# Kernel tuning notes

Hardware: AMD Instinct MI355X
Metric: run time of the kernel (lower is better)

The kernel has to match this reference:

```python
import jax, jax.numpy as jnp
import numpy as np

INPUT_SIZE = 256
OUTPUT_SIZE = 128
N = 8192
SLOPE = 0.01
NEG_BIG = -9e15


def setup_inputs() -> dict:
    key = jax.random.key(0)
    k_h, k_adj, k_W, k_a = jax.random.split(key, 4)
    h = jax.random.normal(k_h, (N, INPUT_SIZE), dtype=jnp.float32)
    adj = jax.random.randint(k_adj, (N, N), 0, 2, dtype=jnp.int32)
    # xavier_uniform with gain=1.414
    gain = 1.414
    lim_W = gain * np.sqrt(6.0 / (INPUT_SIZE + OUTPUT_SIZE))
    W = jax.random.uniform(k_W, (INPUT_SIZE, OUTPUT_SIZE), dtype=jnp.float32, minval=-lim_W, maxval=lim_W)
    lim_a = gain * np.sqrt(6.0 / (2 * OUTPUT_SIZE + 1))
    a = jax.random.uniform(k_a, (2 * OUTPUT_SIZE, 1), dtype=jnp.float32, minval=-lim_a, maxval=lim_a)
    return {"h": h, "adj": adj, "W": W, "a": a}


def reference(h, adj, W, a):
    # Wh: [N, F]
    Wh = h @ W
    Fo = Wh.shape[1]
    # Original builds [N, N, 2F] concat then matmul with a; equivalent to
    # e[i, j] = leaky_relu(Wh[i] . a[:F] + Wh[j] . a[F:]) via broadcasting.
    src = Wh @ a[:Fo, 0]   # [N]
    dst = Wh @ a[Fo:, 0]   # [N]
    e = jax.nn.leaky_relu(src[:, None] + dst[None, :], negative_slope=SLOPE)  # [N, N]
    att = jnp.where(adj > 0, e, NEG_BIG)
    att = jax.nn.softmax(att, axis=1)
    return att @ Wh
```

## Files before the change

kernel.cpp:

```cpp
#include <hip/hip_runtime.h>
#include <hip/hip_bf16.h>

typedef unsigned short u16;
typedef unsigned int u32;
typedef __attribute__((ext_vector_type(8))) short short8;
typedef __attribute__((ext_vector_type(4))) float f32x4;

#define NN 8192
#define KIN 256
#define FOUT 128
#define SPLITS 8
#define KPER (NN / SPLITS)
#define BK 64
#define ITERS (KPER / BK)
#define L2E 1.4426950408889634f

__device__ __forceinline__ float exp2fast(float x) { return __builtin_amdgcn_exp2f(x); }

__device__ __forceinline__ u16 f2bf(float f) {
    u32 u = __float_as_uint(f);
    u32 r = ((u >> 16) & 1u) + 0x7fffu;
    return (u16)((u + r) >> 16);
}
__device__ __forceinline__ u32 pk_bf16(float a, float b) {
    union { __hip_bfloat162 h2; u32 u; } cv;
    cv.h2 = __float22bfloat162_rn(make_float2(a, b));
    return cv.u;
}
__device__ __forceinline__ u32 fkey(float f) {
    u32 b = __float_as_uint(f);
    return (b & 0x80000000u) ? ~b : (b | 0x80000000u);
}
__device__ __forceinline__ float funkey(u32 k) {
    u32 b = (k & 0x80000000u) ? (k & 0x7fffffffu) : ~k;
    return __uint_as_float(b);
}

__global__ __launch_bounds__(256) void k1_wh(
    const float* __restrict__ h, const float* __restrict__ W, const float* __restrict__ a,
    u16* __restrict__ whbt,
    float* __restrict__ src, float* __restrict__ dst, u32* __restrict__ gmaxk)
{
    __shared__ float hT[64][36];
    __shared__ u16   lt[128][40];
    __shared__ float sd[32][2];
    const int t  = threadIdx.x;
    const int m0 = blockIdx.x * 32;
    const int rq = t >> 5, cq = t & 31;

    float acc[4][4];
#pragma unroll
    for (int i = 0; i < 4; i++)
#pragma unroll
        for (int j = 0; j < 4; j++) acc[i][j] = 0.f;
    if (t < 64) sd[t >> 1][t & 1] = 0.f;

    for (int kt = 0; kt < KIN; kt += 64) {
        __syncthreads();
#pragma unroll
        for (int s2 = 0; s2 < 2; s2++) {
            int f = s2 * 256 + t;
            int r = f >> 4, kc = (f & 15) * 4;
            float4 hv = *(const float4*)(h + (size_t)(m0 + r) * KIN + kt + kc);
            hT[kc + 0][r] = hv.x; hT[kc + 1][r] = hv.y;
            hT[kc + 2][r] = hv.z; hT[kc + 3][r] = hv.w;
        }
        __syncthreads();
        for (int k = 0; k < 64; k++) {
            float4 wv = *(const float4*)(W + (size_t)(kt + k) * FOUT + cq * 4);
            float h0 = hT[k][rq * 4 + 0], h1 = hT[k][rq * 4 + 1];
            float h2 = hT[k][rq * 4 + 2], h3 = hT[k][rq * 4 + 3];
            acc[0][0] += h0 * wv.x; acc[0][1] += h0 * wv.y; acc[0][2] += h0 * wv.z; acc[0][3] += h0 * wv.w;
            acc[1][0] += h1 * wv.x; acc[1][1] += h1 * wv.y; acc[1][2] += h1 * wv.z; acc[1][3] += h1 * wv.w;
            acc[2][0] += h2 * wv.x; acc[2][1] += h2 * wv.y; acc[2][2] += h2 * wv.z; acc[2][3] += h2 * wv.w;
            acc[3][0] += h3 * wv.x; acc[3][1] += h3 * wv.y; acc[3][2] += h3 * wv.z; acc[3][3] += h3 * wv.w;
        }
    }
#pragma unroll
    for (int i = 0; i < 4; i++) {
        float sp = 0.f, dp = 0.f;
#pragma unroll
        for (int j = 0; j < 4; j++) {
            sp += acc[i][j] * a[cq * 4 + j];
            dp += acc[i][j] * a[FOUT + cq * 4 + j];
            lt[cq * 4 + j][rq * 4 + i] = f2bf(acc[i][j]);
        }
        atomicAdd(&sd[rq * 4 + i][0], sp);
        atomicAdd(&sd[rq * 4 + i][1], dp);
    }
    __syncthreads();
    if (t < 32) { src[m0 + t] = sd[t][0]; dst[m0 + t] = sd[t][1]; }
    if (t < 64) {
        float v = (t < 32) ? sd[t][1] : -3.0e38f;
#pragma unroll
        for (int off = 32; off >= 1; off >>= 1) v = fmaxf(v, __shfl_down(v, off));
        if (t == 0) atomicMax(gmaxk, fkey(v));
    }
#pragma unroll
    for (int s2 = 0; s2 < 2; s2++) {
        int f = s2 * 256 + t;
        int n = f >> 2;
        int q = (f & 3) * 8;
        uint4 v = *(const uint4*)&lt[n][q];
        *(uint4*)(whbt + (size_t)n * NN + m0 + q) = v;
    }
}

__global__ __launch_bounds__(256, 4) void k2_attn(
    const int* __restrict__ adj, const float* __restrict__ src, const float* __restrict__ dst,
    const u16* __restrict__ whbt, const u32* __restrict__ gmaxk,
    float* __restrict__ accp, float* __restrict__ lp)
{
    __shared__ u16 P[64][72];
    __shared__ u16 Bs[128][72];
    __shared__ float2 sY[64];
    const int t = threadIdx.x;
    const int bx = blockIdx.x;
    const int i0 = bx * 64;
    const int split = blockIdx.y;
    const int kb0 = split * KPER;
    const int lane = t & 63, wave = t >> 6;
    const int nw = wave * 32;
    const int l15 = lane & 15, quad = lane >> 4;
    const int g = t >> 4;
    const int c4 = (t & 15) * 4;

    if (t < 64) {
        float s = src[i0 + t] * L2E;
        float gm = funkey(*gmaxk) * L2E;
        float x = s + gm;
        float C = fmaxf(x, 0.01f * x);
        sY[t] = make_float2(s - C, 0.01f * s - C);
    }
    float psum[4] = {0.f, 0.f, 0.f, 0.f};
    f32x4 acc[4][2];
#pragma unroll
    for (int mt = 0; mt < 4; mt++)
#pragma unroll
        for (int nt = 0; nt < 2; nt++) acc[mt][nt] = {0.f, 0.f, 0.f, 0.f};

    int itc = bx & (ITERS - 1);
    int4 av[4]; float4 d1, d2; uint4 bv[4];
    {
        int kb = kb0 + itc * BK;
        float4 d = *(const float4*)(dst + kb + c4);
        d1 = make_float4(d.x * L2E, d.y * L2E, d.z * L2E, d.w * L2E);
        d2 = make_float4(0.01f * d1.x, 0.01f * d1.y, 0.01f * d1.z, 0.01f * d1.w);
#pragma unroll
        for (int s2 = 0; s2 < 4; s2++)
            av[s2] = *(const int4*)(adj + (size_t)(i0 + 16 * s2 + g) * NN + kb + c4);
#pragma unroll
        for (int p = 0; p < 4; p++) {
            int f = p * 256 + t;
            int n = f >> 3, seg = (f & 7) * 8;
            bv[p] = *(const uint4*)(whbt + (size_t)n * NN + kb + seg);
        }
    }

    for (int it = 0; it < ITERS; ++it) {
        __syncthreads();
#pragma unroll
        for (int s2 = 0; s2 < 4; s2++) {
            int r = 16 * s2 + g;
            float2 y = sY[r];
            int4 a4 = av[s2];
            float x0 = fmaxf(y.x + d1.x, y.y + d2.x);
            float x1 = fmaxf(y.x + d1.y, y.y + d2.y);
            float x2 = fmaxf(y.x + d1.z, y.y + d2.z);
            float x3 = fmaxf(y.x + d1.w, y.y + d2.w);
            x0 = (a4.x > 0) ? x0 : -1.0e9f;
            x1 = (a4.y > 0) ? x1 : -1.0e9f;
            x2 = (a4.z > 0) ? x2 : -1.0e9f;
            x3 = (a4.w > 0) ? x3 : -1.0e9f;
            float p0 = exp2fast(x0), p1 = exp2fast(x1);
            float p2 = exp2fast(x2), p3 = exp2fast(x3);
            psum[s2] += (p0 + p1) + (p2 + p3);
            *(uint2*)&P[r][c4] = make_uint2(pk_bf16(p0, p1), pk_bf16(p2, p3));
        }
#pragma unroll
        for (int p = 0; p < 4; p++) {
            int f = p * 256 + t;
            int n = f >> 3, seg = (f & 7) * 8;
            *(uint4*)&Bs[n][seg] = bv[p];
        }
        __syncthreads();
        if (it + 1 < ITERS) {
            int itn = (itc + 1) & (ITERS - 1);
            int kb = kb0 + itn * BK;
            float4 d = *(const float4*)(dst + kb + c4);
            d1 = make_float4(d.x * L2E, d.y * L2E, d.z * L2E, d.w * L2E);
            d2 = make_float4(0.01f * d1.x, 0.01f * d1.y, 0.01f * d1.z, 0.01f * d1.w);
#pragma unroll
            for (int s2 = 0; s2 < 4; s2++)
                av[s2] = *(const int4*)(adj + (size_t)(i0 + 16 * s2 + g) * NN + kb + c4);
#pragma unroll
            for (int p = 0; p < 4; p++) {
                int f = p * 256 + t;
                int n = f >> 3, seg = (f & 7) * 8;
                bv[p] = *(const uint4*)(whbt + (size_t)n * NN + kb + seg);
            }
            itc = itn;
        }
#pragma unroll
        for (int ks = 0; ks < 2; ks++) {
            int kk = ks * 32 + quad * 8;
            short8 af[4], bfr[2];
#pragma unroll
            for (int mt = 0; mt < 4; mt++)
                af[mt] = *(const short8*)&P[mt * 16 + l15][kk];
#pragma unroll
            for (int nt = 0; nt < 2; nt++)
                bfr[nt] = *(const short8*)&Bs[nw + nt * 16 + l15][kk];
#pragma unroll
            for (int mt = 0; mt < 4; mt++)
#pragma unroll
                for (int nt = 0; nt < 2; nt++)
                    acc[mt][nt] = __builtin_amdgcn_mfma_f32_16x16x32_bf16(
                        af[mt], bfr[nt], acc[mt][nt], 0, 0, 0);
        }
    }
#pragma unroll
    for (int s2 = 0; s2 < 4; s2++) {
        float v = psum[s2];
        v += __shfl_down(v, 8, 16);
        v += __shfl_down(v, 4, 16);
        v += __shfl_down(v, 2, 16);
        v += __shfl_down(v, 1, 16);
        if ((t & 15) == 0) lp[split * NN + i0 + 16 * s2 + g] = v;
    }
    float* ab = accp + (size_t)split * (NN * FOUT);
#pragma unroll
    for (int mt = 0; mt < 4; mt++)
#pragma unroll
        for (int nt = 0; nt < 2; nt++) {
            int tm = bx * 4 + mt;
            int tn = wave * 2 + nt;
            *(f32x4*)&ab[(size_t)(tm * 8 + tn) * 256 + lane * 4] = acc[mt][nt];
        }
}

__global__ __launch_bounds__(256) void k2b_rsum(const float* __restrict__ lp,
                                               float* __restrict__ rinv)
{
    int i = blockIdx.x * 256 + threadIdx.x;
    float s = 0.f;
#pragma unroll
    for (int sp = 0; sp < SPLITS; sp++) s += lp[sp * NN + i];
    rinv[i] = 1.0f / s;
}

__global__ __launch_bounds__(256) void k3_comb(
    const float* __restrict__ accp, const float* __restrict__ rinv, float* __restrict__ out)
{
    int idx = blockIdx.x * 256 + threadIdx.x;
    int tile = idx >> 6, l = idx & 63;
    float4 s = make_float4(0.f, 0.f, 0.f, 0.f);
#pragma unroll
    for (int sp = 0; sp < SPLITS; sp++) {
        float4 v = *(const float4*)(accp + (size_t)sp * (NN * FOUT) + (size_t)idx * 4);
        s.x += v.x; s.y += v.y; s.z += v.z; s.w += v.w;
    }
    int row0 = (tile >> 3) * 16 + (l >> 4) * 4;
    int col  = (tile & 7) * 16 + (l & 15);
    float4 ri = *(const float4*)(rinv + row0);
    out[(size_t)(row0 + 0) * FOUT + col] = s.x * ri.x;
    out[(size_t)(row0 + 1) * FOUT + col] = s.y * ri.y;
    out[(size_t)(row0 + 2) * FOUT + col] = s.z * ri.z;
    out[(size_t)(row0 + 3) * FOUT + col] = s.w * ri.w;
}

extern "C" void kernel_launch(void* const* d_in, const int* in_sizes, int n_in,
                              void* d_out, int out_size, void* d_ws, size_t ws_size,
                              hipStream_t stream) {
    const float* h   = (const float*)d_in[0];
    const int*   adj = (const int*)d_in[1];
    const float* W   = (const float*)d_in[2];
    const float* a   = (const float*)d_in[3];
    float* out = (float*)d_out;

    char* ws = (char*)d_ws;
    u16*   whbt  = (u16*)ws;
    float* src   = (float*)(ws + (2u << 20));
    float* dst   = src + NN;
    u32*   gmaxk = (u32*)(dst + NN);
    float* accp  = (float*)(ws + (3u << 20));
    float* lp    = (float*)(ws + (35u << 20));
    float* rinv  = (float*)(ws + (36u << 20));

    (void)hipMemsetAsync(gmaxk, 0, sizeof(u32), stream);
    k1_wh<<<dim3(NN / 32), dim3(256), 0, stream>>>(h, W, a, whbt, src, dst, gmaxk);
    k2_attn<<<dim3(NN / 64, SPLITS), dim3(256), 0, stream>>>(adj, src, dst, whbt, gmaxk, accp, lp);
    k2b_rsum<<<dim3(NN / 256), dim3(256), 0, stream>>>(lp, rinv);
    k3_comb<<<dim3((NN * FOUT / 4) / 256), dim3(256), 0, stream>>>(accp, rinv, out);
}
```

Before: 470.8 us.

## Store Wh in MFMA fragment layout and compute attention per-wave without LDS

k1 now writes Wh as pre-swizzled bf16 MFMA B-fragments, so each lane can load its operand directly from global memory. k2 drops the shared-memory P and B tiles and both barriers. Each wave owns a 16-row strip, computes the masked exp probabilities in registers as its A fragment, and issues 8 MFMAs over all 128 output columns per 32-wide K step, with a two-step register prefetch of adj and dst. The intent is to remove LDS traffic and synchronisation. The cost is that Wh fragments are reloaded from global/L2 by every wave instead of being shared through LDS within a block.

```diff
diff --git a/kernel.cpp b/kernel.cpp
--- a/kernel.cpp
+++ b/kernel.cpp
@@ -11,8 +11,7 @@
 #define FOUT 128
 #define SPLITS 8
 #define KPER (NN / SPLITS)
-#define BK 64
-#define ITERS (KPER / BK)
+#define KSTEPS (KPER / 32)
 #define L2E 1.4426950408889634f
 
 __device__ __forceinline__ float exp2fast(float x) { return __builtin_amdgcn_exp2f(x); }
@@ -38,8 +37,8 @@
 
 __global__ __launch_bounds__(256) void k1_wh(
     const float* __restrict__ h, const float* __restrict__ W, const float* __restrict__ a,
-    u16* __restrict__ whbt,
-    float* __restrict__ src, float* __restrict__ dst, u32* __restrict__ gmaxk)
+    u16* __restrict__ whfrag,
+    float* __restrict__ src, float* __restrict__ dl2e, u32* __restrict__ gmaxk)
 {
     __shared__ float hT[64][36];
     __shared__ u16   lt[128][40];
@@ -89,154 +88,116 @@
         atomicAdd(&sd[rq * 4 + i][1], dp);
     }
     __syncthreads();
-    if (t < 32) { src[m0 + t] = sd[t][0]; dst[m0 + t] = sd[t][1]; }
+    if (t < 32) { src[m0 + t] = sd[t][0]; dl2e[m0 + t] = sd[t][1] * L2E; }
     if (t < 64) {
         float v = (t < 32) ? sd[t][1] : -3.0e38f;
 #pragma unroll
         for (int off = 32; off >= 1; off >>= 1) v = fmaxf(v, __shfl_down(v, off));
         if (t == 0) atomicMax(gmaxk, fkey(v));
     }
-#pragma unroll
-    for (int s2 = 0; s2 < 2; s2++) {
-        int f = s2 * 256 + t;
-        int n = f >> 2;
-        int q = (f & 3) * 8;
-        uint4 v = *(const uint4*)&lt[n][q];
-        *(uint4*)(whbt + (size_t)n * NN + m0 + q) = v;
+    const int kstep = blockIdx.x;
+#pragma unroll
+    for (int p = 0; p < 2; p++) {
+        int f = p * 256 + t;
+        int nt = f >> 6;
+        int l  = f & 63;
+        short8 v = *(const short8*)&lt[nt * 16 + (l & 15)][(l >> 4) * 8];
+        *(short8*)(whfrag + ((size_t)(kstep * 8 + nt) * 64 + l) * 8) = v;
     }
 }
 
 __global__ __launch_bounds__(256, 4) void k2_attn(
-    const int* __restrict__ adj, const float* __restrict__ src, const float* __restrict__ dst,
-    const u16* __restrict__ whbt, const u32* __restrict__ gmaxk,
+    const int* __restrict__ adj, const float* __restrict__ src, const float* __restrict__ dl2e,
+    const u16* __restrict__ whfrag, const u32* __restrict__ gmaxk,
     float* __restrict__ accp, float* __restrict__ lp)
 {
-    __shared__ u16 P[64][72];
-    __shared__ u16 Bs[128][72];
-    __shared__ float2 sY[64];
     const int t = threadIdx.x;
-    const int bx = blockIdx.x;
-    const int i0 = bx * 64;
+    const int lane = t & 63, wave = t >> 6;
+    const int strip = blockIdx.x * 4 + wave;
+    const int i0 = strip * 16;
     const int split = blockIdx.y;
-    const int kb0 = split * KPER;
-    const int lane = t & 63, wave = t >> 6;
-    const int nw = wave * 32;
-    const int l15 = lane & 15, quad = lane >> 4;
-    const int g = t >> 4;
-    const int c4 = (t & 15) * 4;
-
-    if (t < 64) {
-        float s = src[i0 + t] * L2E;
-        float gm = funkey(*gmaxk) * L2E;
-        float x = s + gm;
-        float C = fmaxf(x, 0.01f * x);
-        sY[t] = make_float2(s - C, 0.01f * s - C);
-    }
-    float psum[4] = {0.f, 0.f, 0.f, 0.f};
-    f32x4 acc[4][2];
-#pragma unroll
-    for (int mt = 0; mt < 4; mt++)
-#pragma unroll
-        for (int nt = 0; nt < 2; nt++) acc[mt][nt] = {0.f, 0.f, 0.f, 0.f};
-
-    int itc = bx & (ITERS - 1);
-    int4 av[4]; float4 d1, d2; uint4 bv[4];
-    {
-        int kb = kb0 + itc * BK;
-        float4 d = *(const float4*)(dst + kb + c4);
-        d1 = make_float4(d.x * L2E, d.y * L2E, d.z * L2E, d.w * L2E);
-        d2 = make_float4(0.01f * d1.x, 0.01f * d1.y, 0.01f * d1.z, 0.01f * d1.w);
-#pragma unroll
-        for (int s2 = 0; s2 < 4; s2++)
-            av[s2] = *(const int4*)(adj + (size_t)(i0 + 16 * s2 + g) * NN + kb + c4);
-#pragma unroll
-        for (int p = 0; p < 4; p++) {
-            int f = p * 256 + t;
-            int n = f >> 3, seg = (f & 7) * 8;
-            bv[p] = *(const uint4*)(whbt + (size_t)n * NN + kb + seg);
-        }
-    }
-
-    for (int it = 0; it < ITERS; ++it) {
-        __syncthreads();
-#pragma unroll
-        for (int s2 = 0; s2 < 4; s2++) {
-            int r = 16 * s2 + g;
-            float2 y = sY[r];
-            int4 a4 = av[s2];
-            float x0 = fmaxf(y.x + d1.x, y.y + d2.x);
-            float x1 = fmaxf(y.x + d1.y, y.y + d2.y);
-            float x2 = fmaxf(y.x + d1.z, y.y + d2.z);
-            float x3 = fmaxf(y.x + d1.w, y.y + d2.w);
-            x0 = (a4.x > 0) ? x0 : -1.0e9f;
-            x1 = (a4.y > 0) ? x1 : -1.0e9f;
-            x2 = (a4.z > 0) ? x2 : -1.0e9f;
-            x3 = (a4.w > 0) ? x3 : -1.0e9f;
-            float p0 = exp2fast(x0), p1 = exp2fast(x1);
-            float p2 = exp2fast(x2), p3 = exp2fast(x3);
-            psum[s2] += (p0 + p1) + (p2 + p3);
-            *(uint2*)&P[r][c4] = make_uint2(pk_bf16(p0, p1), pk_bf16(p2, p3));
-        }
-#pragma unroll
-        for (int p = 0; p < 4; p++) {
-            int f = p * 256 + t;
-            int n = f >> 3, seg = (f & 7) * 8;
-            *(uint4*)&Bs[n][seg] = bv[p];
-        }
-        __syncthreads();
-        if (it + 1 < ITERS) {
-            int itn = (itc + 1) & (ITERS - 1);
-            int kb = kb0 + itn * BK;
-            float4 d = *(const float4*)(dst + kb + c4);
-            d1 = make_float4(d.x * L2E, d.y * L2E, d.z * L2E, d.w * L2E);
-            d2 = make_float4(0.01f * d1.x, 0.01f * d1.y, 0.01f * d1.z, 0.01f * d1.w);
-#pragma unroll
-            for (int s2 = 0; s2 < 4; s2++)
-                av[s2] = *(const int4*)(adj + (size_t)(i0 + 16 * s2 + g) * NN + kb + c4);
-#pragma unroll
-            for (int p = 0; p < 4; p++) {
-                int f = p * 256 + t;
-                int n = f >> 3, seg = (f & 7) * 8;
-                bv[p] = *(const uint4*)(whbt + (size_t)n * NN + kb + seg);
-            }
-            itc = itn;
-        }
-#pragma unroll
-        for (int ks = 0; ks < 2; ks++) {
-            int kk = ks * 32 + quad * 8;
-            short8 af[4], bfr[2];
-#pragma unroll
-            for (int mt = 0; mt < 4; mt++)
-                af[mt] = *(const short8*)&P[mt * 16 + l15][kk];
-#pragma unroll
-            for (int nt = 0; nt < 2; nt++)
-                bfr[nt] = *(const short8*)&Bs[nw + nt * 16 + l15][kk];
-#pragma unroll
-            for (int mt = 0; mt < 4; mt++)
-#pragma unroll
-                for (int nt = 0; nt < 2; nt++)
-                    acc[mt][nt] = __builtin_amdgcn_mfma_f32_16x16x32_bf16(
-                        af[mt], bfr[nt], acc[mt][nt], 0, 0, 0);
-        }
-    }
-#pragma unroll
-    for (int s2 = 0; s2 < 4; s2++) {
-        float v = psum[s2];
-        v += __shfl_down(v, 8, 16);
-        v += __shfl_down(v, 4, 16);
-        v += __shfl_down(v, 2, 16);
-        v += __shfl_down(v, 1, 16);
-        if ((t & 15) == 0) lp[split * NN + i0 + 16 * s2 + g] = v;
-    }
+    const int l15 = lane & 15;
+    const int kq = (lane >> 4) * 8;
+
+    float sp = src[i0 + l15] * L2E;
+    float gm = funkey(*gmaxk) * L2E;
+    float xx = sp + gm;
+    float C = fmaxf(xx, 0.01f * xx);
+    const float y1 = sp - C, y2 = 0.01f * sp - C;
+
+    const int* arow = adj + (size_t)(i0 + l15) * NN;
+    const int st0 = blockIdx.x & (KSTEPS - 1);
+    const int kbase = split * KPER;
+
+    f32x4 acc[8];
+#pragma unroll
+    for (int nt = 0; nt < 8; nt++) acc[nt] = {0.f, 0.f, 0.f, 0.f};
+    float psum = 0.f;
+
+    int4 aL[2], aH[2]; float4 dL[2], dH[2];
+#pragma unroll
+    for (int s = 0; s < 2; s++) {
+        int kb = kbase + ((st0 + s) & (KSTEPS - 1)) * 32;
+        aL[s] = *(const int4*)(arow + kb + kq);
+        aH[s] = *(const int4*)(arow + kb + kq + 4);
+        dL[s] = *(const float4*)(dl2e + kb + kq);
+        dH[s] = *(const float4*)(dl2e + kb + kq + 4);
+    }
+
+#pragma unroll 4
+    for (int it = 0; it < KSTEPS; ++it) {
+        const int sl = it & 1;
+        const int kb = kbase + ((st0 + it) & (KSTEPS - 1)) * 32;
+
+        uint4 bv[8];
+        const u16* wf = whfrag + ((size_t)(kb >> 5) * 8 * 64 + lane) * 8;
+#pragma unroll
+        for (int nt = 0; nt < 8; nt++)
+            bv[nt] = *(const uint4*)(wf + (size_t)nt * 64 * 8);
+
+        int4 al = aL[sl], ah = aH[sl];
+        float4 dl = dL[sl], dh = dH[sl];
+        float p0, p1, p2, p3, p4, p5, p6, p7;
+        {
+            float x;
+            x = fmaxf(y1 + dl.x, y2 + 0.01f * dl.x); p0 = exp2fast(al.x > 0 ? x : -1.0e9f);
+            x = fmaxf(y1 + dl.y, y2 + 0.01f * dl.y); p1 = exp2fast(al.y > 0 ? x : -1.0e9f);
+            x = fmaxf(y1 + dl.z, y2 + 0.01f * dl.z); p2 = exp2fast(al.z > 0 ? x : -1.0e9f);
+            x = fmaxf(y1 + dl.w, y2 + 0.01f * dl.w); p3 = exp2fast(al.w > 0 ? x : -1.0e9f);
+            x = fmaxf(y1 + dh.x, y2 + 0.01f * dh.x); p4 = exp2fast(ah.x > 0 ? x : -1.0e9f);
+            x = fmaxf(y1 + dh.y, y2 + 0.01f * dh.y); p5 = exp2fast(ah.y > 0 ? x : -1.0e9f);
+            x = fmaxf(y1 + dh.z, y2 + 0.01f * dh.z); p6 = exp2fast(ah.z > 0 ? x : -1.0e9f);
+            x = fmaxf(y1 + dh.w, y2 + 0.01f * dh.w); p7 = exp2fast(ah.w > 0 ? x : -1.0e9f);
+        }
+        psum += ((p0 + p1) + (p2 + p3)) + ((p4 + p5) + (p6 + p7));
+        union { short8 s8; u32 u[4]; } af;
+        af.u[0] = pk_bf16(p0, p1); af.u[1] = pk_bf16(p2, p3);
+        af.u[2] = pk_bf16(p4, p5); af.u[3] = pk_bf16(p6, p7);
+
+        {
+            int kb2 = kbase + ((st0 + it + 2) & (KSTEPS - 1)) * 32;
+            aL[sl] = *(const int4*)(arow + kb2 + kq);
+            aH[sl] = *(const int4*)(arow + kb2 + kq + 4);
+            dL[sl] = *(const float4*)(dl2e + kb2 + kq);
+            dH[sl] = *(const float4*)(dl2e + kb2 + kq + 4);
+        }
+
+#pragma unroll
+        for (int nt = 0; nt < 8; nt++) {
+            union { uint4 q; short8 s8; } bf; bf.q = bv[nt];
+            acc[nt] = __builtin_amdgcn_mfma_f32_16x16x32_bf16(af.s8, bf.s8, acc[nt], 0, 0, 0);
+        }
+    }
+
+    float v = psum;
+    v += __shfl_down(v, 32);
+    v += __shfl_down(v, 16);
+    if (lane < 16) lp[split * NN + i0 + lane] = v;
+
     float* ab = accp + (size_t)split * (NN * FOUT);
 #pragma unroll
-    for (int mt = 0; mt < 4; mt++)
-#pragma unroll
-        for (int nt = 0; nt < 2; nt++) {
-            int tm = bx * 4 + mt;
-            int tn = wave * 2 + nt;
-            *(f32x4*)&ab[(size_t)(tm * 8 + tn) * 256 + lane * 4] = acc[mt][nt];
-        }
+    for (int nt = 0; nt < 8; nt++)
+        *(f32x4*)&ab[((size_t)(strip * 8 + nt) * 64 + lane) * 4] = acc[nt];
 }
 
 __global__ __launch_bounds__(256) void k2b_rsum(const float* __restrict__ lp,
@@ -279,17 +240,17 @@
     float* out = (float*)d_out;
 
     char* ws = (char*)d_ws;
-    u16*   whbt  = (u16*)ws;
-    float* src   = (float*)(ws + (2u << 20));
-    float* dst   = src + NN;
-    u32*   gmaxk = (u32*)(dst + NN);
-    float* accp  = (float*)(ws + (3u << 20));
-    float* lp    = (float*)(ws + (35u << 20));
-    float* rinv  = (float*)(ws + (36u << 20));
+    u16*   whfrag = (u16*)ws;
+    float* src    = (float*)(ws + (2u << 20));
+    float* dl2e   = src + NN;
+    u32*   gmaxk  = (u32*)(dl2e + NN);
+    float* accp   = (float*)(ws + (3u << 20));
+    float* lp     = (float*)(ws + (35u << 20));
+    float* rinv   = (float*)(ws + (36u << 20));
 
     (void)hipMemsetAsync(gmaxk, 0, sizeof(u32), stream);
-    k1_wh<<<dim3(NN / 32), dim3(256), 0, stream>>>(h, W, a, whbt, src, dst, gmaxk);
-    k2_attn<<<dim3(NN / 64, SPLITS), dim3(256), 0, stream>>>(adj, src, dst, whbt, gmaxk, accp, lp);
+    k1_wh<<<dim3(NN / 32), dim3(256), 0, stream>>>(h, W, a, whfrag, src, dl2e, gmaxk);
+    k2_attn<<<dim3(NN / 64, SPLITS), dim3(256), 0, stream>>>(adj, src, dl2e, whfrag, gmaxk, accp, lp);
     k2b_rsum<<<dim3(NN / 256), dim3(256), 0, stream>>>(lp, rinv);
     k3_comb<<<dim3((NN * FOUT / 4) / 256), dim3(256), 0, stream>>>(accp, rinv, out);
 }
```

Measured after the change: 445.8 us. 5.3% less time.
